# Kernel tuning notes

Hardware: AMD Instinct MI355X
Metric: run time of the kernel (lower is better)

## Reference

```python
import jax, jax.numpy as jnp
import numpy as np

IMAGE_SIZE = 256
SIGMA = 1.0   # soft-rasterization sharpness (pixels)
EPS = 1e-8


def _quat_to_rot(q):
    q = q / jnp.sqrt(jnp.sum(q * q) + EPS)
    w, x, y, z = q[0], q[1], q[2], q[3]
    return jnp.stack([
        jnp.stack([1 - 2 * (y * y + z * z), 2 * (x * y - w * z), 2 * (x * z + w * y)]),
        jnp.stack([2 * (x * y + w * z), 1 - 2 * (x * x + z * z), 2 * (y * z - w * x)]),
        jnp.stack([2 * (x * z - w * y), 2 * (y * z + w * x), 1 - 2 * (x * x + y * y)]),
    ])


def _render_silhouette(vertices, faces, q, t, K):
    # camera transform: v_cam = R(q) v + t   [V,3]
    R = _quat_to_rot(q)
    vc = vertices[0] @ R.T + t
    z = vc[:, 2] + EPS
    # perspective projection to pixel coords
    px_v = K[0, 0] * vc[:, 0] / z + K[0, 2]
    py_v = K[1, 1] * vc[:, 1] / z + K[1, 2]
    verts2d = jnp.stack([px_v, py_v], axis=-1)          # [V,2]
    tri = verts2d[faces[0]]                             # [F,3,2]

    e01 = tri[:, 1] - tri[:, 0]
    e02 = tri[:, 2] - tri[:, 0]
    area2 = e01[:, 0] * e02[:, 1] - e01[:, 1] * e02[:, 0]
    s = jnp.where(area2 >= 0, 1.0, -1.0)                # [F]

    # pixel centers
    ii, jj = jnp.meshgrid(jnp.arange(IMAGE_SIZE), jnp.arange(IMAGE_SIZE), indexing='ij')
    px = (jj.astype(jnp.float32) + 0.5).reshape(-1)     # [P]
    py = (ii.astype(jnp.float32) + 0.5).reshape(-1)     # [P]

    # signed distance to triangle = min over edges of normalized edge function
    d = None
    for k in range(3):
        a = tri[:, k]
        b = tri[:, (k + 1) % 3]
        ex = b[:, 0] - a[:, 0]
        ey = b[:, 1] - a[:, 1]
        inv_len = s / jnp.sqrt(ex * ex + ey * ey + EPS)  # sign folded in
        cx = -ey * inv_len
        cy = ex * inv_len
        c0 = (ey * a[:, 0] - ex * a[:, 1]) * inv_len
        c = px[:, None] * cx[None, :] + py[:, None] * cy[None, :] + c0[None, :]  # [P,F]
        d = c if d is None else jnp.minimum(d, c)

    # soft coverage: alpha = 1 - prod_F (1 - sigmoid(d/sigma))
    log_not_cov = jax.nn.log_sigmoid(-d / SIGMA)         # [P,F]
    sil = 1.0 - jnp.exp(jnp.sum(log_not_cov, axis=1))    # [P]
    return sil.reshape(IMAGE_SIZE, IMAGE_SIZE)


def setup_inputs() -> dict:
    key = jax.random.key(0)
    k1, k2, k3 = jax.random.split(key, 3)
    V, F = 1000, 1000
    vertices = jax.random.normal(k1, (1, V, 3), jnp.float32) * 0.3
    faces = jax.random.randint(k2, (1, F, 3), 0, V, jnp.int32)
    image_ref = jax.random.uniform(k3, (IMAGE_SIZE, IMAGE_SIZE), dtype=jnp.float32)
    q = jnp.array([1.0, 0.05, -0.03, 0.02], dtype=jnp.float32)
    t = jnp.array([0.0, 0.0, 2.732], dtype=jnp.float32)
    K = jnp.array([[280.0, 0.0, 128.0], [0.0, 280.0, 128.0], [0.0, 0.0, 1.0]], dtype=jnp.float32)
    return {"vertices": vertices, "faces": faces, "q": q, "t": t, "K": K, "image_ref": image_ref}


def reference(vertices, faces, q, t, K, image_ref):
    image = _render_silhouette(vertices, faces, q, t, K)   # [256,256]
    loss = jnp.mean((image - image_ref) ** 2, axis=1)      # per-row mean, [256]
    return loss
```

## Files before the change

kernel.cpp:

```cpp
#include <hip/hip_runtime.h>
#include <math.h>

#define IMG 256
#define NFACE 1000
#define NFP 1024
#define NWAVE 4
#define EPSF 1e-8f
#define LOG2E 1.44269504088896f
#define TCUT 16.0f
#define ACC_BREAK 25.0f
#define CULL_M (-(TCUT + 7.15f))

__device__ float g_soa[9][NFP];
__device__ float4 g_cf[NFP * 3];

__global__ __launch_bounds__(256) void k_coeff(const float* __restrict__ verts,
                                               const int* __restrict__ faces,
                                               const float* __restrict__ q,
                                               const float* __restrict__ t,
                                               const float* __restrict__ K,
                                               float* __restrict__ out) {
    int f = blockIdx.x * 256 + threadIdx.x;
    if (blockIdx.x == 0 && threadIdx.x < IMG) out[threadIdx.x] = 0.f;
    if (f >= NFP) return;

    float c[9];
    if (f < NFACE) {
        float qw = q[0], qx = q[1], qy = q[2], qz = q[3];
        float qn = sqrtf(qw * qw + qx * qx + qy * qy + qz * qz + EPSF);
        qw /= qn; qx /= qn; qy /= qn; qz /= qn;
        float R00 = 1.f - 2.f * (qy * qy + qz * qz);
        float R01 = 2.f * (qx * qy - qw * qz);
        float R02 = 2.f * (qx * qz + qw * qy);
        float R10 = 2.f * (qx * qy + qw * qz);
        float R11 = 1.f - 2.f * (qx * qx + qz * qz);
        float R12 = 2.f * (qy * qz - qw * qx);
        float R20 = 2.f * (qx * qz - qw * qy);
        float R21 = 2.f * (qy * qz + qw * qx);
        float R22 = 1.f - 2.f * (qx * qx + qy * qy);
        float tx = t[0], ty = t[1], tz = t[2];
        float K00 = K[0], K02 = K[2], K11 = K[4], K12 = K[5];

        float X[3], Y[3];
#pragma unroll
        for (int k = 0; k < 3; ++k) {
            int vi = faces[f * 3 + k];
            float vx = verts[vi * 3 + 0];
            float vy = verts[vi * 3 + 1];
            float vz = verts[vi * 3 + 2];
            float cx = R00 * vx + R01 * vy + R02 * vz + tx;
            float cy = R10 * vx + R11 * vy + R12 * vz + ty;
            float cz = R20 * vx + R21 * vy + R22 * vz + tz;
            float z = cz + EPSF;
            X[k] = K00 * cx / z + K02;
            Y[k] = K11 * cy / z + K12;
        }

        float e01x = X[1] - X[0], e01y = Y[1] - Y[0];
        float e02x = X[2] - X[0], e02y = Y[2] - Y[0];
        float area2 = e01x * e02y - e01y * e02x;
        float s = (area2 >= 0.f) ? LOG2E : -LOG2E;

#pragma unroll
        for (int k = 0; k < 3; ++k) {
            int k1 = (k + 1) % 3;
            float ex = X[k1] - X[k];
            float ey = Y[k1] - Y[k];
            float inv = s / sqrtf(ex * ex + ey * ey + EPSF);
            c[k * 3 + 0] = -ey * inv;
            c[k * 3 + 1] = ex * inv;
            c[k * 3 + 2] = (ey * X[k] - ex * Y[k]) * inv;
        }
    } else {
        c[0] = 0.f; c[1] = 0.f; c[2] = -1e9f;
        c[3] = 0.f; c[4] = 0.f; c[5] = -1e9f;
        c[6] = 0.f; c[7] = 0.f; c[8] = -1e9f;
    }

#pragma unroll
    for (int k = 0; k < 9; ++k) g_soa[k][f] = c[k];
    g_cf[f * 3 + 0] = make_float4(c[0], c[1], c[2], 0.f);
    g_cf[f * 3 + 1] = make_float4(c[3], c[4], c[5], 0.f);
    g_cf[f * 3 + 2] = make_float4(c[6], c[7], c[8], 0.f);
}

__global__ __launch_bounds__(256) void k_main(const float* __restrict__ image_ref,
                                              float* __restrict__ out) {
    const int tid = threadIdx.x;
    const int wave = tid >> 6;
    const int lane = tid & 63;
    const int x0 = blockIdx.x * 8, y0 = blockIdx.y * 8;
    const int col = x0 + (lane & 7);
    const int row = y0 + (lane >> 3);
    const float px = col + 0.5f;
    const float py = row + 0.5f;
    const float tcx = x0 + 4.0f;
    const float tcy = y0 + 4.0f;

    __shared__ __align__(8) short s_list[NWAVE][260];
    __shared__ float s_acc[NWAVE][64];

    const int wbase = wave * 256;
    int cnt = 0;
#pragma unroll
    for (int r = 0; r < 4; ++r) {
        int f = wbase + r * 64 + lane;
        float a0 = g_soa[0][f], a1 = g_soa[1][f], a2 = g_soa[2][f];
        float b0 = g_soa[3][f], b1 = g_soa[4][f], b2 = g_soa[5][f];
        float d0 = g_soa[6][f], d1 = g_soa[7][f], d2 = g_soa[8][f];
        float m = fminf(fminf(fmaf(tcx, a0, fmaf(tcy, a1, a2)),
                              fmaf(tcx, b0, fmaf(tcy, b1, b2))),
                        fmaf(tcx, d0, fmaf(tcy, d1, d2)));
        bool hit = (m > CULL_M);
        unsigned long long msk = __ballot(hit);
        if (hit) {
            int pos = __popcll(msk & ((1ull << lane) - 1ull));
            s_list[wave][cnt + pos] = (short)f;
        }
        cnt += __popcll(msk);
    }
    int cntp = (cnt + 3) & ~3;
    if (lane < cntp - cnt) s_list[wave][cnt + lane] = (short)NFACE;

    float acc = 0.f;
    for (int i = 0; i < cntp; i += 4) {
        short4 id = *(const short4*)&s_list[wave][i];
        const float4* pA = &g_cf[id.x * 3];
        const float4* pB = &g_cf[id.y * 3];
        const float4* pC = &g_cf[id.z * 3];
        const float4* pD = &g_cf[id.w * 3];
        float4 aA = pA[0], bA = pA[1], cA = pA[2];
        float4 aB = pB[0], bB = pB[1], cB = pB[2];
        float4 aC = pC[0], bC = pC[1], cC = pC[2];
        float4 aD = pD[0], bD = pD[1], cD = pD[2];
        float uA = fminf(fminf(fmaf(px, aA.x, fmaf(py, aA.y, aA.z)),
                               fmaf(px, bA.x, fmaf(py, bA.y, bA.z))),
                         fmaf(px, cA.x, fmaf(py, cA.y, cA.z)));
        float uB = fminf(fminf(fmaf(px, aB.x, fmaf(py, aB.y, aB.z)),
                               fmaf(px, bB.x, fmaf(py, bB.y, bB.z))),
                         fmaf(px, cB.x, fmaf(py, cB.y, cB.z)));
        float uC = fminf(fminf(fmaf(px, aC.x, fmaf(py, aC.y, aC.z)),
                               fmaf(px, bC.x, fmaf(py, bC.y, bC.z))),
                         fmaf(px, cC.x, fmaf(py, cC.y, cC.z)));
        float uD = fminf(fminf(fmaf(px, aD.x, fmaf(py, aD.y, aD.z)),
                               fmaf(px, bD.x, fmaf(py, bD.y, bD.z))),
                         fmaf(px, cD.x, fmaf(py, cD.y, cD.z)));
        acc += fmaxf(uA, 0.f) + fmaxf(uB, 0.f) + fmaxf(uC, 0.f) + fmaxf(uD, 0.f);
        acc += __builtin_amdgcn_logf(1.f + __builtin_amdgcn_exp2f(-fabsf(uA)));
        acc += __builtin_amdgcn_logf(1.f + __builtin_amdgcn_exp2f(-fabsf(uB)));
        acc += __builtin_amdgcn_logf(1.f + __builtin_amdgcn_exp2f(-fabsf(uC)));
        acc += __builtin_amdgcn_logf(1.f + __builtin_amdgcn_exp2f(-fabsf(uD)));
        if (__all(acc > ACC_BREAK)) break;
    }

    s_acc[wave][lane] = acc;
    __syncthreads();
    if (wave == 0) {
        float tot = s_acc[0][lane] + s_acc[1][lane] +
                    s_acc[2][lane] + s_acc[3][lane];
        float sil = 1.f - __builtin_amdgcn_exp2f(-tot);
        float d = sil - image_ref[row * IMG + col];
        float v = d * d;
        v += __shfl_xor(v, 1);
        v += __shfl_xor(v, 2);
        v += __shfl_xor(v, 4);
        if ((lane & 7) == 0) atomicAdd(&out[row], v * (1.f / 256.f));
    }
}

extern "C" void kernel_launch(void* const* d_in, const int* in_sizes, int n_in,
                              void* d_out, int out_size, void* d_ws, size_t ws_size,
                              hipStream_t stream) {
    const float* verts = (const float*)d_in[0];
    const int* faces = (const int*)d_in[1];
    const float* q = (const float*)d_in[2];
    const float* t = (const float*)d_in[3];
    const float* K = (const float*)d_in[4];
    const float* image_ref = (const float*)d_in[5];
    float* out = (float*)d_out;

    k_coeff<<<NFP / 256, 256, 0, stream>>>(verts, faces, q, t, K, out);
    k_main<<<dim3(IMG / 8, IMG / 8), 256, 0, stream>>>(image_ref, out);
}
```

Before: 24.44 us.

## Replace LDS face list and gathers with register readlane broadcast of culled faces

Drops the shared-memory compacted face list and the float4 global gather table. Each wave now keeps the face coefficients it loaded in registers, iterates over the ballot mask with ffs, and broadcasts each hit face's nine coefficients via readlane to every lane. This removes the LDS writes and the scattered global loads, but processes one face per iteration with a serial scalar dependency instead of four independent faces. The early break is now checked only after each 64-face chunk rather than every four faces.

```diff
diff --git a/kernel.cpp b/kernel.cpp
--- a/kernel.cpp
+++ b/kernel.cpp
@@ -12,7 +12,10 @@
 #define CULL_M (-(TCUT + 7.15f))
 
 __device__ float g_soa[9][NFP];
-__device__ float4 g_cf[NFP * 3];
+
+__device__ __forceinline__ float bcast(float x, int s) {
+    return __uint_as_float(__builtin_amdgcn_readlane(__float_as_uint(x), s));
+}
 
 __global__ __launch_bounds__(256) void k_coeff(const float* __restrict__ verts,
                                                const int* __restrict__ faces,
@@ -79,9 +82,6 @@
 
 #pragma unroll
     for (int k = 0; k < 9; ++k) g_soa[k][f] = c[k];
-    g_cf[f * 3 + 0] = make_float4(c[0], c[1], c[2], 0.f);
-    g_cf[f * 3 + 1] = make_float4(c[3], c[4], c[5], 0.f);
-    g_cf[f * 3 + 2] = make_float4(c[6], c[7], c[8], 0.f);
 }
 
 __global__ __launch_bounds__(256) void k_main(const float* __restrict__ image_ref,
@@ -97,59 +97,31 @@
     const float tcx = x0 + 4.0f;
     const float tcy = y0 + 4.0f;
 
-    __shared__ __align__(8) short s_list[NWAVE][260];
     __shared__ float s_acc[NWAVE][64];
 
+    float acc = 0.f;
     const int wbase = wave * 256;
-    int cnt = 0;
-#pragma unroll
     for (int r = 0; r < 4; ++r) {
-        int f = wbase + r * 64 + lane;
-        float a0 = g_soa[0][f], a1 = g_soa[1][f], a2 = g_soa[2][f];
-        float b0 = g_soa[3][f], b1 = g_soa[4][f], b2 = g_soa[5][f];
-        float d0 = g_soa[6][f], d1 = g_soa[7][f], d2 = g_soa[8][f];
-        float m = fminf(fminf(fmaf(tcx, a0, fmaf(tcy, a1, a2)),
-                              fmaf(tcx, b0, fmaf(tcy, b1, b2))),
-                        fmaf(tcx, d0, fmaf(tcy, d1, d2)));
-        bool hit = (m > CULL_M);
-        unsigned long long msk = __ballot(hit);
-        if (hit) {
-            int pos = __popcll(msk & ((1ull << lane) - 1ull));
-            s_list[wave][cnt + pos] = (short)f;
+        const int f = wbase + r * 64 + lane;
+        float l0 = g_soa[0][f], l1 = g_soa[1][f], l2 = g_soa[2][f];
+        float l3 = g_soa[3][f], l4 = g_soa[4][f], l5 = g_soa[5][f];
+        float l6 = g_soa[6][f], l7 = g_soa[7][f], l8 = g_soa[8][f];
+        float m = fminf(fminf(fmaf(tcx, l0, fmaf(tcy, l1, l2)),
+                              fmaf(tcx, l3, fmaf(tcy, l4, l5))),
+                        fmaf(tcx, l6, fmaf(tcy, l7, l8)));
+        unsigned long long msk = __ballot(m > CULL_M);
+        while (msk) {
+            int s = __ffsll((unsigned long long)msk) - 1;
+            msk &= msk - 1;
+            float a0 = bcast(l0, s), a1 = bcast(l1, s), a2 = bcast(l2, s);
+            float b0 = bcast(l3, s), b1 = bcast(l4, s), b2 = bcast(l5, s);
+            float c0 = bcast(l6, s), c1 = bcast(l7, s), c2 = bcast(l8, s);
+            float u = fminf(fminf(fmaf(px, a0, fmaf(py, a1, a2)),
+                                  fmaf(px, b0, fmaf(py, b1, b2))),
+                            fmaf(px, c0, fmaf(py, c1, c2)));
+            acc += fmaxf(u, 0.f);
+            acc += __builtin_amdgcn_logf(1.f + __builtin_amdgcn_exp2f(-fabsf(u)));
         }
-        cnt += __popcll(msk);
-    }
-    int cntp = (cnt + 3) & ~3;
-    if (lane < cntp - cnt) s_list[wave][cnt + lane] = (short)NFACE;
-
-    float acc = 0.f;
-    for (int i = 0; i < cntp; i += 4) {
-        short4 id = *(const short4*)&s_list[wave][i];
-        const float4* pA = &g_cf[id.x * 3];
-        const float4* pB = &g_cf[id.y * 3];
-        const float4* pC = &g_cf[id.z * 3];
-        const float4* pD = &g_cf[id.w * 3];
-        float4 aA = pA[0], bA = pA[1], cA = pA[2];
-        float4 aB = pB[0], bB = pB[1], cB = pB[2];
-        float4 aC = pC[0], bC = pC[1], cC = pC[2];
-        float4 aD = pD[0], bD = pD[1], cD = pD[2];
-        float uA = fminf(fminf(fmaf(px, aA.x, fmaf(py, aA.y, aA.z)),
-                               fmaf(px, bA.x, fmaf(py, bA.y, bA.z))),
-                         fmaf(px, cA.x, fmaf(py, cA.y, cA.z)));
-        float uB = fminf(fminf(fmaf(px, aB.x, fmaf(py, aB.y, aB.z)),
-                               fmaf(px, bB.x, fmaf(py, bB.y, bB.z))),
-                         fmaf(px, cB.x, fmaf(py, cB.y, cB.z)));
-        float uC = fminf(fminf(fmaf(px, aC.x, fmaf(py, aC.y, aC.z)),
-                               fmaf(px, bC.x, fmaf(py, bC.y, bC.z))),
-                         fmaf(px, cC.x, fmaf(py, cC.y, cC.z)));
-        float uD = fminf(fminf(fmaf(px, aD.x, fmaf(py, aD.y, aD.z)),
-                               fmaf(px, bD.x, fmaf(py, bD.y, bD.z))),
-                         fmaf(px, cD.x, fmaf(py, cD.y, cD.z)));
-        acc += fmaxf(uA, 0.f) + fmaxf(uB, 0.f) + fmaxf(uC, 0.f) + fmaxf(uD, 0.f);
-        acc += __builtin_amdgcn_logf(1.f + __builtin_amdgcn_exp2f(-fabsf(uA)));
-        acc += __builtin_amdgcn_logf(1.f + __builtin_amdgcn_exp2f(-fabsf(uB)));
-        acc += __builtin_amdgcn_logf(1.f + __builtin_amdgcn_exp2f(-fabsf(uC)));
-        acc += __builtin_amdgcn_logf(1.f + __builtin_amdgcn_exp2f(-fabsf(uD)));
         if (__all(acc > ACC_BREAK)) break;
     }
 
```

Result: faster. 21.22 us (-13.2%).
